# Kernel optimization log

Hardware: AMD Instinct MI355X
Metric: run time of the kernel (lower is better)

Reference implementation:

```python
import jax, jax.numpy as jnp
import numpy as np

IN_C, HID_C, OUT_C = 602, 256, 41
N_SRC0, N_TGT0, N_TGT1 = 256000, 10240, 1024
E0, E1 = 256000, 10240


def setup_inputs() -> dict:
    key = jax.random.key(0)
    ks = jax.random.split(key, 12)
    x = jax.random.normal(ks[0], (N_SRC0, IN_C), dtype=jnp.float32)
    src0 = jax.random.randint(ks[1], (E0,), 0, N_SRC0, dtype=jnp.int32)
    dst0 = jax.random.randint(ks[2], (E0,), 0, N_TGT0, dtype=jnp.int32)
    src1 = jax.random.randint(ks[3], (E1,), 0, N_TGT0, dtype=jnp.int32)
    dst1 = jax.random.randint(ks[4], (E1,), 0, N_TGT1, dtype=jnp.int32)
    s1 = 1.0 / np.sqrt(IN_C)
    s2 = 1.0 / np.sqrt(HID_C)
    Wl1 = jax.random.uniform(ks[5], (IN_C, HID_C), jnp.float32, -s1, s1)
    Wr1 = jax.random.uniform(ks[6], (IN_C, HID_C), jnp.float32, -s1, s1)
    b1 = jnp.zeros((HID_C,), jnp.float32)
    Wl2 = jax.random.uniform(ks[7], (HID_C, OUT_C), jnp.float32, -s2, s2)
    Wr2 = jax.random.uniform(ks[8], (HID_C, OUT_C), jnp.float32, -s2, s2)
    b2 = jnp.zeros((OUT_C,), jnp.float32)
    return {"x": x, "src0": src0, "dst0": dst0, "src1": src1, "dst1": dst1,
            "Wl1": Wl1, "Wr1": Wr1, "b1": b1, "Wl2": Wl2, "Wr2": Wr2, "b2": b2,
            "n_tgt0": N_TGT0, "n_tgt1": N_TGT1}


def _sage_conv(x_src, x_tgt, src, dst, Wl, Wr, b, n_tgt):
    # mean aggregation of source messages per target node (0 for isolated targets)
    msg = x_src[src]                                                   # [E, C]
    ssum = jax.ops.segment_sum(msg, dst, num_segments=n_tgt)           # [n_tgt, C]
    cnt = jax.ops.segment_sum(jnp.ones((src.shape[0], 1), x_src.dtype), dst,
                              num_segments=n_tgt)
    agg = ssum / jnp.maximum(cnt, 1.0)
    return agg @ Wl + x_tgt @ Wr + b


def reference(x, src0, dst0, src1, dst1, Wl1, Wr1, b1, Wl2, Wr2, b2, n_tgt0, n_tgt1):
    # layer 1: bipartite SAGEConv, x_target = x[:n_tgt0]
    h = _sage_conv(x, x[:n_tgt0], src0, dst0, Wl1, Wr1, b1, n_tgt0)
    h = jax.nn.relu(h)  # dropout omitted (eval / deterministic)
    # layer 2
    out = _sage_conv(h, h[:n_tgt1], src1, dst1, Wl2, Wr2, b2, n_tgt1)
    return jax.nn.log_softmax(out, axis=-1)
```

## Files before the change

kernel.cpp:

```cpp
#include <hip/hip_runtime.h>
#include <hip/hip_bf16.h>

#define IN_C   602
#define HID_C  256
#define OUT_C  41
#define N_TGT0 10240
#define N_TGT1 1024
#define E0     256000
#define E1     10240
#define KTOT   1216
#define NWK    (HID_C * KTOT)

typedef unsigned short u16;
typedef __attribute__((ext_vector_type(4))) float f32x4;
typedef __attribute__((ext_vector_type(8))) short bf16x8;

__device__ __forceinline__ u16 f2bf(float v) {
    union { float f; unsigned u; } c; c.f = v;
    unsigned u = c.u;
    u += 0x7fffu + ((u >> 16) & 1u);
    return (u16)(u >> 16);
}
__device__ __forceinline__ float bf2f(u16 v) {
    union { unsigned u; float f; } c; c.u = ((unsigned)v) << 16; return c.f;
}

__device__ __forceinline__ void gload16(const void* g, void* l) {
    __builtin_amdgcn_global_load_lds(
        (const __attribute__((address_space(1))) void*)g,
        (__attribute__((address_space(3))) void*)l, 16, 0, 0);
}

__global__ __launch_bounds__(256) void build_kernel(
    const int* __restrict__ src0, const int* __restrict__ dst0,
    const int* __restrict__ src1, const int* __restrict__ dst1,
    int* __restrict__ head0, int* __restrict__ next0,
    int* __restrict__ head1, int* __restrict__ next1,
    const float* __restrict__ Wl, const float* __restrict__ Wr, u16* __restrict__ BT)
{
    int id = blockIdx.x * 256 + threadIdx.x;
    if (id < E0) {
        int p = atomicExch(&head0[dst0[id]], id);
        next0[id] = p;
    } else if (id < E0 + E1) {
        int e = id - E0;
        int p = atomicExch(&head1[dst1[e]], e);
        next1[e] = p;
    }
    if (id < NWK) {
        int n = id / KTOT, k = id - n * KTOT;
        float v = 0.f;
        if (k < IN_C)                        v = Wl[(size_t)k * HID_C + n];
        else if (k >= 608 && k < 608 + IN_C) v = Wr[(size_t)(k - 608) * HID_C + n];
        BT[id] = f2bf(v);
    }
}

__global__ __launch_bounds__(256) void agg0_ll(
    const float* __restrict__ x, const int* __restrict__ head,
    const int* __restrict__ next, const int* __restrict__ srcv,
    u16* __restrict__ A)
{
    int t = blockIdx.x * 4 + (threadIdx.x >> 6);
    int lane = threadIdx.x & 63;

    float2 a0 = make_float2(0.f, 0.f), a1 = a0, a2 = a0, a3 = a0, a4 = a0;
    int d = 0;

    int cur = head[t];
    int s   = (cur >= 0) ? srcv[cur] : 0;
    int nxt = (cur >= 0) ? next[cur] : -1;
    while (cur >= 0) {
        const float2* r = (const float2*)(x + (size_t)s * IN_C);
        float2 v0 = r[lane], v1 = r[lane + 64], v2 = r[lane + 128], v3 = r[lane + 192];
        int curN = nxt;
        int sN   = (curN >= 0) ? srcv[curN] : 0;
        int nxtN = (curN >= 0) ? next[curN] : -1;
        a0.x += v0.x; a0.y += v0.y;
        a1.x += v1.x; a1.y += v1.y;
        a2.x += v2.x; a2.y += v2.y;
        a3.x += v3.x; a3.y += v3.y;
        if (lane < 45) {
            float2 v4 = r[lane + 256];
            a4.x += v4.x; a4.y += v4.y;
        }
        ++d;
        cur = curN; s = sN; nxt = nxtN;
    }

    float inv = 1.0f / (float)(d > 1 ? d : 1);
    ushort2* orow = (ushort2*)(A + (size_t)t * KTOT);
    ushort2 o;
    o.x = f2bf(a0.x * inv); o.y = f2bf(a0.y * inv); orow[lane]       = o;
    o.x = f2bf(a1.x * inv); o.y = f2bf(a1.y * inv); orow[lane + 64]  = o;
    o.x = f2bf(a2.x * inv); o.y = f2bf(a2.y * inv); orow[lane + 128] = o;
    o.x = f2bf(a3.x * inv); o.y = f2bf(a3.y * inv); orow[lane + 192] = o;
    if (lane < 45) {
        o.x = f2bf(a4.x * inv); o.y = f2bf(a4.y * inv); orow[lane + 256] = o;
    } else if (lane < 48) {
        o.x = 0; o.y = 0; orow[lane + 256] = o;
    }

    const float2* xt = (const float2*)(x + (size_t)t * IN_C);
    ushort2* orow2 = orow + 304;
    float2 w0 = xt[lane], w1 = xt[lane + 64], w2 = xt[lane + 128], w3 = xt[lane + 192];
    o.x = f2bf(w0.x); o.y = f2bf(w0.y); orow2[lane]       = o;
    o.x = f2bf(w1.x); o.y = f2bf(w1.y); orow2[lane + 64]  = o;
    o.x = f2bf(w2.x); o.y = f2bf(w2.y); orow2[lane + 128] = o;
    o.x = f2bf(w3.x); o.y = f2bf(w3.y); orow2[lane + 192] = o;
    if (lane < 45) {
        float2 w4 = xt[lane + 256];
        o.x = f2bf(w4.x); o.y = f2bf(w4.y); orow2[lane + 256] = o;
    } else if (lane < 48) {
        o.x = 0; o.y = 0; orow2[lane + 256] = o;
    }
}

#define GBM 64
#define GBN 64
#define GBK 64
#define GNIT (KTOT / GBK)

__global__ __launch_bounds__(256) void gemm1_tile(
    const u16* __restrict__ A, const u16* __restrict__ BT,
    const float* __restrict__ bias, u16* __restrict__ h)
{
    __shared__ __align__(16) u16 As[2][GBM * GBK];
    __shared__ __align__(16) u16 Bs[2][GBN * GBK];
    int tid = threadIdx.x;
    int w = tid >> 6, lane = tid & 63;
    int d = blockIdx.x;
    int ni = (d >> 3) & 3;
    int mi = (d & 7) + ((d >> 5) << 3);
    int bm = mi * GBM, bn = ni * GBN;

    int r16 = lane & 15;
    int g = lane >> 4;
    int wm2 = w >> 1, wn2 = w & 1;

    int srow = lane >> 3;
    int sslot = (lane & 7) ^ srow;
    const u16* gA0 = A  + (size_t)(bm + w * 16 + srow) * KTOT + sslot * 8;
    const u16* gA1 = gA0 + (size_t)8 * KTOT;
    const u16* gB0 = BT + (size_t)(bn + w * 16 + srow) * KTOT + sslot * 8;
    const u16* gB1 = gB0 + (size_t)8 * KTOT;

    int xr = r16 & 7;
    int rowA0 = wm2 * 32 + r16;
    int rowB0 = wn2 * 32 + r16;

    f32x4 acc[2][2] = {};

    auto stage = [&](int buf, int k0) {
        u16* dA = &As[buf][w * 1024];
        u16* dB = &Bs[buf][w * 1024];
        gload16(gA0 + k0, dA);
        gload16(gA1 + k0, dA + 512);
        gload16(gB0 + k0, dB);
        gload16(gB1 + k0, dB + 512);
    };

    stage(0, 0);
    __syncthreads();

    int cur = 0;
    for (int it = 0; it < GNIT; ++it) {
        if (it + 1 < GNIT) stage(cur ^ 1, (it + 1) * GBK);

        #pragma unroll
        for (int ks = 0; ks < 2; ++ks) {
            int sl = ((ks << 2) + g);
            bf16x8 a0 = *(const bf16x8*)(&As[cur][rowA0 * 64 + ((sl ^ xr) << 3)]);
            bf16x8 a1 = *(const bf16x8*)(&As[cur][(rowA0 + 16) * 64 + ((sl ^ xr) << 3)]);
            bf16x8 b0 = *(const bf16x8*)(&Bs[cur][rowB0 * 64 + ((sl ^ xr) << 3)]);
            bf16x8 b1 = *(const bf16x8*)(&Bs[cur][(rowB0 + 16) * 64 + ((sl ^ xr) << 3)]);
            acc[0][0] = __builtin_amdgcn_mfma_f32_16x16x32_bf16(a0, b0, acc[0][0], 0, 0, 0);
            acc[0][1] = __builtin_amdgcn_mfma_f32_16x16x32_bf16(a0, b1, acc[0][1], 0, 0, 0);
            acc[1][0] = __builtin_amdgcn_mfma_f32_16x16x32_bf16(a1, b0, acc[1][0], 0, 0, 0);
            acc[1][1] = __builtin_amdgcn_mfma_f32_16x16x32_bf16(a1, b1, acc[1][1], 0, 0, 0);
        }
        __syncthreads();
        cur ^= 1;
    }

    int row4 = g * 4;
    #pragma unroll
    for (int fn = 0; fn < 2; ++fn) {
        int n = bn + wn2 * 32 + fn * 16 + r16;
        float b = bias[n];
        #pragma unroll
        for (int fm = 0; fm < 2; ++fm) {
            #pragma unroll
            for (int j = 0; j < 4; ++j) {
                int m = bm + wm2 * 32 + fm * 16 + row4 + j;
                float v = acc[fm][fn][j] + b;
                h[(size_t)m * HID_C + n] = f2bf(v > 0.f ? v : 0.f);
            }
        }
    }
}

__global__ __launch_bounds__(64) void out_fused(
    const u16* __restrict__ h, const int* __restrict__ head,
    const int* __restrict__ next, const int* __restrict__ srcv,
    const float* __restrict__ Wl, const float* __restrict__ Wr,
    const float* __restrict__ bias, float* __restrict__ out)
{
    __shared__ float arow[HID_C];
    __shared__ float hrow[HID_C];
    int t = blockIdx.x;
    int lane = threadIdx.x;

    float4 acc = make_float4(0.f, 0.f, 0.f, 0.f);
    int d = 0;
    int cur = head[t];
    int s   = (cur >= 0) ? srcv[cur] : 0;
    int nxt = (cur >= 0) ? next[cur] : -1;
    while (cur >= 0) {
        ushort4 v = ((const ushort4*)(h + (size_t)s * HID_C))[lane];
        int curN = nxt;
        int sN   = (curN >= 0) ? srcv[curN] : 0;
        int nxtN = (curN >= 0) ? next[curN] : -1;
        acc.x += bf2f(v.x); acc.y += bf2f(v.y);
        acc.z += bf2f(v.z); acc.w += bf2f(v.w);
        ++d;
        cur = curN; s = sN; nxt = nxtN;
    }
    float inv = 1.0f / (float)(d > 1 ? d : 1);
    ((float4*)arow)[lane] = make_float4(acc.x * inv, acc.y * inv, acc.z * inv, acc.w * inv);
    ushort4 hv = ((const ushort4*)(h + (size_t)t * HID_C))[lane];
    ((float4*)hrow)[lane] = make_float4(bf2f(hv.x), bf2f(hv.y), bf2f(hv.z), bf2f(hv.w));
    __syncthreads();

    float v = 0.f;
    if (lane < OUT_C) {
        v = bias[lane];
        for (int k = 0; k < HID_C; ++k)
            v += arow[k] * Wl[k * OUT_C + lane] + hrow[k] * Wr[k * OUT_C + lane];
    }
    float m = (lane < OUT_C) ? v : -1e30f;
    #pragma unroll
    for (int off = 32; off; off >>= 1) m = fmaxf(m, __shfl_xor(m, off));
    float ex = (lane < OUT_C) ? expf(v - m) : 0.f;
    float sum = ex;
    #pragma unroll
    for (int off = 32; off; off >>= 1) sum += __shfl_xor(sum, off);
    float lse = m + logf(sum);
    if (lane < OUT_C) out[(size_t)t * OUT_C + lane] = v - lse;
}


extern "C" void kernel_launch(void* const* d_in, const int* in_sizes, int n_in,
                              void* d_out, int out_size, void* d_ws, size_t ws_size,
                              hipStream_t stream) {
    const float* x    = (const float*)d_in[0];
    const int*   src0 = (const int*)d_in[1];
    const int*   dst0 = (const int*)d_in[2];
    const int*   src1 = (const int*)d_in[3];
    const int*   dst1 = (const int*)d_in[4];
    const float* Wl1  = (const float*)d_in[5];
    const float* Wr1  = (const float*)d_in[6];
    const float* b1   = (const float*)d_in[7];
    const float* Wl2  = (const float*)d_in[8];
    const float* Wr2  = (const float*)d_in[9];
    const float* b2   = (const float*)d_in[10];
    float* out = (float*)d_out;

    char* ws = (char*)d_ws;
    size_t off = 0;
    auto take = [&](size_t bytes) { void* p = ws + off; off += (bytes + 255) & ~(size_t)255; return p; };
    u16* A     = (u16*)take((size_t)N_TGT0 * KTOT * 2);
    u16* BT    = (u16*)take((size_t)HID_C * KTOT * 2);
    u16* h     = (u16*)take((size_t)N_TGT0 * HID_C * 2);
    int* head0 = (int*)take((size_t)(N_TGT0 + N_TGT1) * 4);
    int* head1 = head0 + N_TGT0;
    int* next0 = (int*)take((size_t)E0 * 4);
    int* next1 = (int*)take((size_t)E1 * 4);

    hipMemsetAsync(head0, 0xFF, (size_t)(N_TGT0 + N_TGT1) * sizeof(int), stream);

    build_kernel<<<(NWK + 255) / 256, 256, 0, stream>>>(
        src0, dst0, src1, dst1, head0, next0, head1, next1, Wl1, Wr1, BT);

    agg0_ll<<<N_TGT0 / 4, 256, 0, stream>>>(x, head0, next0, src0, A);

    gemm1_tile<<<640, 256, 0, stream>>>(A, BT, b1, h);

    out_fused<<<N_TGT1, 64, 0, stream>>>(h, head1, next1, src1, Wl2, Wr2, b2, out);
}
```

Before: 186.0 us.

## Phase neighbor gathers by source-row range for cache locality; use nontemporal stores

The aggregation kernel now first walks each target's linked list and stashes up to 128 source indices in lane registers. It then makes 8 passes, each gathering only the sources whose index falls in one 32768-row slice of x (sj>>15). Running all waves in roughly the same phase at the same time is meant to keep the gathered rows of the 616 MB x in L2/MALL. Output rows are written with nontemporal stores so they do not evict cached x. This adds extra loop iterations and shuffles per phase and depends on waves staying roughly in step across phases.

```diff
diff --git a/kernel.cpp b/kernel.cpp
--- a/kernel.cpp
+++ b/kernel.cpp
@@ -10,6 +10,7 @@
 #define E1     10240
 #define KTOT   1216
 #define NWK    (HID_C * KTOT)
+#define NPHASE 8
 
 typedef unsigned short u16;
 typedef __attribute__((ext_vector_type(4))) float f32x4;
@@ -23,6 +24,10 @@
 }
 __device__ __forceinline__ float bf2f(u16 v) {
     union { unsigned u; float f; } c; c.u = ((unsigned)v) << 16; return c.f;
+}
+__device__ __forceinline__ void ntstore_u2(ushort2 v, ushort2* p) {
+    unsigned u = (unsigned)v.x | ((unsigned)v.y << 16);
+    __builtin_nontemporal_store(u, (unsigned*)p);
 }
 
 __device__ __forceinline__ void gload16(const void* g, void* l) {
@@ -56,7 +61,7 @@
     }
 }
 
-__global__ __launch_bounds__(256) void agg0_ll(
+__global__ __launch_bounds__(256) void agg0_phased(
     const float* __restrict__ x, const int* __restrict__ head,
     const int* __restrict__ next, const int* __restrict__ srcv,
     u16* __restrict__ A)
@@ -66,53 +71,81 @@
 
     float2 a0 = make_float2(0.f, 0.f), a1 = a0, a2 = a0, a3 = a0, a4 = a0;
     int d = 0;
+    int my0 = 0, my1 = 0;
 
     int cur = head[t];
     int s   = (cur >= 0) ? srcv[cur] : 0;
     int nxt = (cur >= 0) ? next[cur] : -1;
     while (cur >= 0) {
-        const float2* r = (const float2*)(x + (size_t)s * IN_C);
-        float2 v0 = r[lane], v1 = r[lane + 64], v2 = r[lane + 128], v3 = r[lane + 192];
         int curN = nxt;
         int sN   = (curN >= 0) ? srcv[curN] : 0;
         int nxtN = (curN >= 0) ? next[curN] : -1;
-        a0.x += v0.x; a0.y += v0.y;
-        a1.x += v1.x; a1.y += v1.y;
-        a2.x += v2.x; a2.y += v2.y;
-        a3.x += v3.x; a3.y += v3.y;
-        if (lane < 45) {
-            float2 v4 = r[lane + 256];
-            a4.x += v4.x; a4.y += v4.y;
+        if (d < 64) {
+            if (lane == d) my0 = s;
+        } else if (d < 128) {
+            if (lane == d - 64) my1 = s;
+        } else {
+            const float2* r = (const float2*)(x + (size_t)s * IN_C);
+            float2 v0 = r[lane], v1 = r[lane + 64], v2 = r[lane + 128], v3 = r[lane + 192];
+            a0.x += v0.x; a0.y += v0.y;
+            a1.x += v1.x; a1.y += v1.y;
+            a2.x += v2.x; a2.y += v2.y;
+            a3.x += v3.x; a3.y += v3.y;
+            if (lane < 45) {
+                float2 v4 = r[lane + 256];
+                a4.x += v4.x; a4.y += v4.y;
+            }
         }
         ++d;
         cur = curN; s = sN; nxt = nxtN;
+    }
+
+    {
+        const float2* xt = (const float2*)(x + (size_t)t * IN_C);
+        ushort2* orow2 = (ushort2*)(A + (size_t)t * KTOT) + 304;
+        ushort2 o;
+        float2 w0 = xt[lane], w1 = xt[lane + 64], w2 = xt[lane + 128], w3 = xt[lane + 192];
+        o.x = f2bf(w0.x); o.y = f2bf(w0.y); ntstore_u2(o, orow2 + lane);
+        o.x = f2bf(w1.x); o.y = f2bf(w1.y); ntstore_u2(o, orow2 + lane + 64);
+        o.x = f2bf(w2.x); o.y = f2bf(w2.y); ntstore_u2(o, orow2 + lane + 128);
+        o.x = f2bf(w3.x); o.y = f2bf(w3.y); ntstore_u2(o, orow2 + lane + 192);
+        if (lane < 45) {
+            float2 w4 = xt[lane + 256];
+            o.x = f2bf(w4.x); o.y = f2bf(w4.y); ntstore_u2(o, orow2 + lane + 256);
+        } else if (lane < 48) {
+            o.x = 0; o.y = 0; ntstore_u2(o, orow2 + lane + 256);
+        }
+    }
+
+    int dcap = d < 128 ? d : 128;
+    for (int p = 0; p < NPHASE; ++p) {
+        for (int j = 0; j < dcap; ++j) {
+            int sj = __shfl((j < 64) ? my0 : my1, j & 63);
+            if ((sj >> 15) != p) continue;
+            const float2* r = (const float2*)(x + (size_t)sj * IN_C);
+            float2 v0 = r[lane], v1 = r[lane + 64], v2 = r[lane + 128], v3 = r[lane + 192];
+            a0.x += v0.x; a0.y += v0.y;
+            a1.x += v1.x; a1.y += v1.y;
+            a2.x += v2.x; a2.y += v2.y;
+            a3.x += v3.x; a3.y += v3.y;
+            if (lane < 45) {
+                float2 v4 = r[lane + 256];
+                a4.x += v4.x; a4.y += v4.y;
+            }
+        }
     }
 
     float inv = 1.0f / (float)(d > 1 ? d : 1);
     ushort2* orow = (ushort2*)(A + (size_t)t * KTOT);
     ushort2 o;
-    o.x = f2bf(a0.x * inv); o.y = f2bf(a0.y * inv); orow[lane]       = o;
-    o.x = f2bf(a1.x * inv); o.y = f2bf(a1.y * inv); orow[lane + 64]  = o;
-    o.x = f2bf(a2.x * inv); o.y = f2bf(a2.y * inv); orow[lane + 128] = o;
-    o.x = f2bf(a3.x * inv); o.y = f2bf(a3.y * inv); orow[lane + 192] = o;
+    o.x = f2bf(a0.x * inv); o.y = f2bf(a0.y * inv); ntstore_u2(o, orow + lane);
+    o.x = f2bf(a1.x * inv); o.y = f2bf(a1.y * inv); ntstore_u2(o, orow + lane + 64);
+    o.x = f2bf(a2.x * inv); o.y = f2bf(a2.y * inv); ntstore_u2(o, orow + lane + 128);
+    o.x = f2bf(a3.x * inv); o.y = f2bf(a3.y * inv); ntstore_u2(o, orow + lane + 192);
     if (lane < 45) {
-        o.x = f2bf(a4.x * inv); o.y = f2bf(a4.y * inv); orow[lane + 256] = o;
+        o.x = f2bf(a4.x * inv); o.y = f2bf(a4.y * inv); ntstore_u2(o, orow + lane + 256);
     } else if (lane < 48) {
-        o.x = 0; o.y = 0; orow[lane + 256] = o;
-    }
-
-    const float2* xt = (const float2*)(x + (size_t)t * IN_C);
-    ushort2* orow2 = orow + 304;
-    float2 w0 = xt[lane], w1 = xt[lane + 64], w2 = xt[lane + 128], w3 = xt[lane + 192];
-    o.x = f2bf(w0.x); o.y = f2bf(w0.y); orow2[lane]       = o;
-    o.x = f2bf(w1.x); o.y = f2bf(w1.y); orow2[lane + 64]  = o;
-    o.x = f2bf(w2.x); o.y = f2bf(w2.y); orow2[lane + 128] = o;
-    o.x = f2bf(w3.x); o.y = f2bf(w3.y); orow2[lane + 192] = o;
-    if (lane < 45) {
-        float2 w4 = xt[lane + 256];
-        o.x = f2bf(w4.x); o.y = f2bf(w4.y); orow2[lane + 256] = o;
-    } else if (lane < 48) {
-        o.x = 0; o.y = 0; orow2[lane + 256] = o;
+        o.x = 0; o.y = 0; ntstore_u2(o, orow + lane + 256);
     }
 }
 
@@ -282,7 +315,7 @@
     build_kernel<<<(NWK + 255) / 256, 256, 0, stream>>>(
         src0, dst0, src1, dst1, head0, next0, head1, next1, Wl1, Wr1, BT);
 
-    agg0_ll<<<N_TGT0 / 4, 256, 0, stream>>>(x, head0, next0, src0, A);
+    agg0_phased<<<N_TGT0 / 4, 256, 0, stream>>>(x, head0, next0, src0, A);
 
     gemm1_tile<<<640, 256, 0, stream>>>(A, BT, b1, h);
 
```

After: 211.0 us. 1.13x slower.
